# Performance work log

Measured on AMD Instinct MI355X. Metric: run time of the kernel, lower is better.

Reference implementation:

```python
import jax, jax.numpy as jnp
import numpy as np

D_MODEL = 1024
NUM_HEADS = 16
D_K = D_MODEL // NUM_HEADS
THETA = 10000.0


def apply_rope(x, positions):
    # x: [b, h, s, d_k]; positions: [b, s] int32
    half = D_K // 2
    inv_freq = THETA ** (-jnp.arange(half, dtype=jnp.float32) * 2.0 / D_K)  # [half]
    angles = positions[:, None, :, None].astype(jnp.float32) * inv_freq  # [b,1,s,half]
    cos, sin = jnp.cos(angles), jnp.sin(angles)
    x1 = x[..., 0::2]  # even dims
    x2 = x[..., 1::2]  # odd dims
    out_even = x1 * cos - x2 * sin
    out_odd = x1 * sin + x2 * cos
    # re-interleave
    out = jnp.stack([out_even, out_odd], axis=-1)
    return out.reshape(x.shape)


def setup_inputs() -> dict:
    key = jax.random.key(0)
    ks = jax.random.split(key, 5)
    b, s = 2, 2048
    scale = 0.02
    return {
        "x": jax.random.normal(ks[0], (b, s, D_MODEL), dtype=jnp.float32),
        "Wq": jax.random.normal(ks[1], (D_MODEL, D_MODEL), dtype=jnp.float32) * scale,
        "Wk": jax.random.normal(ks[2], (D_MODEL, D_MODEL), dtype=jnp.float32) * scale,
        "Wv": jax.random.normal(ks[3], (D_MODEL, D_MODEL), dtype=jnp.float32) * scale,
        "Wo": jax.random.normal(ks[4], (D_MODEL, D_MODEL), dtype=jnp.float32) * scale,
    }


def reference(x, Wq, Wk, Wv, Wo):
    b, s, _ = x.shape
    # Linear(d, d) applied as x @ W^T (torch Linear convention, no bias)
    Q = x @ Wq.T
    K = x @ Wk.T
    V = x @ Wv.T
    # split heads: [b, s, h*d] -> [b, h, s, d]
    split = lambda t: t.reshape(b, s, NUM_HEADS, D_K).transpose(0, 2, 1, 3)
    Q, K, V = split(Q), split(K), split(V)
    positions = jnp.broadcast_to(jnp.arange(s, dtype=jnp.int32), (b, s))
    Q = apply_rope(Q, positions)
    K = apply_rope(K, positions)
    scores = jnp.einsum('bhqd,bhkd->bhqk', Q, K) / jnp.sqrt(jnp.float32(D_K))
    causal = jnp.tril(jnp.ones((s, s), dtype=bool))
    scores = jnp.where(causal[None, None], scores, -jnp.inf)
    attn = jax.nn.softmax(scores, axis=-1)
    out = jnp.einsum('bhqk,bhkd->bhqd', attn, V)
    out = out.transpose(0, 2, 1, 3).reshape(b, s, D_MODEL)
    return out @ Wo.T
```

## Files before the change

kernel.cpp:

```cpp
#include <hip/hip_runtime.h>

typedef __attribute__((ext_vector_type(8))) short bf16x8;
typedef __attribute__((ext_vector_type(4))) float f32x4;
typedef __attribute__((ext_vector_type(16))) float f32x16;

typedef const __attribute__((address_space(1))) unsigned int gu32;
typedef __attribute__((address_space(3))) unsigned int lu32;

__device__ __forceinline__ void async16(const void* g, void* l) {
  __builtin_amdgcn_global_load_lds((gu32*)g, (lu32*)l, 16, 0, 0);
}

__device__ __forceinline__ unsigned short f2bf(float f) {
  unsigned int u = __float_as_uint(f);
  u += 0x7fffu + ((u >> 16) & 1u);
  return (unsigned short)(u >> 16);
}
__device__ __forceinline__ float b2f(unsigned short s) {
  return __uint_as_float(((unsigned int)s) << 16);
}
__device__ __forceinline__ unsigned int cvtpk(float lo, float hi) {
  unsigned int w;
  asm("v_cvt_pk_bf16_f32 %0, %1, %2" : "=v"(w) : "v"(lo), "v"(hi));
  return w;
}
__device__ __forceinline__ void plswap(unsigned int& x, unsigned int& y) {
  asm("v_permlane32_swap_b32 %0, %1" : "+v"(x), "+v"(y));
}

__global__ __launch_bounds__(256) void cvt_k(const float* __restrict__ in,
                                             unsigned short* __restrict__ out,
                                             int n4) {
  int i = blockIdx.x * 256 + threadIdx.x;
  if (i >= n4) return;
  float4 v = ((const float4*)in)[i];
  ushort4 o;
  o.x = f2bf(v.x); o.y = f2bf(v.y); o.z = f2bf(v.z); o.w = f2bf(v.w);
  ((ushort4*)out)[i] = o;
}

template <int WRITE_F32>
__global__ __launch_bounds__(256) void gemm_bt(const unsigned short* __restrict__ A,
                                               const unsigned short* __restrict__ B,
                                               void* __restrict__ Cp, int N, int K) {
  __shared__ __align__(16) unsigned short Al[128 * 64];
  __shared__ __align__(16) unsigned short Bl[128 * 64];
  const int t = threadIdx.x;
  const int w = t >> 6, l = t & 63;
  const int wm = w >> 1, wn = w & 1;
  const int lr = l & 15, lg = l >> 4;
  const long bm = (long)blockIdx.x * 128, bn = (long)blockIdx.y * 128;
  const int srow = t >> 3, scol = (t & 7) * 8;
  f32x4 acc[4][4] = {};
  for (int k0 = 0; k0 < K; k0 += 64) {
    __syncthreads();
    #pragma unroll
    for (int r = 0; r < 4; ++r) {
      int row = r * 32 + srow;
      async16(&A[(bm + row) * (long)K + k0 + scol], &Al[row * 64 + scol]);
      async16(&B[(bn + row) * (long)K + k0 + scol], &Bl[row * 64 + scol]);
    }
    __syncthreads();
    #pragma unroll
    for (int ks = 0; ks < 2; ++ks) {
      bf16x8 af[4], bf[4];
      #pragma unroll
      for (int i = 0; i < 4; ++i) {
        af[i] = *(const bf16x8*)&Al[(wm * 64 + i * 16 + lr) * 64 + ks * 32 + lg * 8];
        bf[i] = *(const bf16x8*)&Bl[(wn * 64 + i * 16 + lr) * 64 + ks * 32 + lg * 8];
      }
      #pragma unroll
      for (int i = 0; i < 4; ++i)
        #pragma unroll
        for (int j = 0; j < 4; ++j)
          acc[i][j] = __builtin_amdgcn_mfma_f32_16x16x32_bf16(af[i], bf[j], acc[i][j], 0, 0, 0);
    }
  }
  #pragma unroll
  for (int i = 0; i < 4; ++i)
    #pragma unroll
    for (int j = 0; j < 4; ++j)
      #pragma unroll
      for (int r = 0; r < 4; ++r) {
        long row = bm + wm * 64 + i * 16 + lg * 4 + r;
        long col = bn + wn * 64 + j * 16 + lr;
        float v = acc[i][j][r];
        if (WRITE_F32) ((float*)Cp)[row * N + col] = v;
        else ((unsigned short*)Cp)[row * N + col] = f2bf(v);
      }
}

__global__ __launch_bounds__(256) void rope_k(unsigned short* __restrict__ QKV) {
  int idx = blockIdx.x * 256 + threadIdx.x;
  int row = idx >> 9;
  int rem = idx & 511;
  int h = rem >> 5;
  int i = rem & 31;
  int s = row & 2047;
  float invf = exp2f((float)i * (-13.287712379549449f / 32.0f));
  float ang = (float)s * invf;
  float sn, cs;
  sincosf(ang, &sn, &cs);
  size_t base = (size_t)row * 3072 + h * 64 + 2 * i;
  #pragma unroll
  for (int qk = 0; qk < 2; ++qk) {
    size_t off = base + (size_t)qk * 1024;
    float x1 = b2f(QKV[off]);
    float x2 = b2f(QKV[off + 1]);
    QKV[off]     = f2bf(x1 * cs - x2 * sn);
    QKV[off + 1] = f2bf(x1 * sn + x2 * cs);
  }
}

__global__ __launch_bounds__(256) void vtr_k(const unsigned short* __restrict__ QKV,
                                             unsigned short* __restrict__ Vt) {
  __shared__ unsigned short tl[64][66];
  const int kt = blockIdx.x;
  const int bh = blockIdx.y;
  const int b = bh >> 4, h = bh & 15;
  const int t = threadIdx.x;
  const int row = t >> 3, c8 = t & 7;
  #pragma unroll
  for (int r = 0; r < 2; ++r) {
    int k = r * 32 + row;
    bf16x8 v = *(const bf16x8*)&QKV[((long)b * 2048 + kt * 64 + k) * 3072 + 2048 + h * 64 + c8 * 8];
    #pragma unroll
    for (int j = 0; j < 8; ++j) tl[c8 * 8 + j][k] = (unsigned short)v[j];
  }
  __syncthreads();
  #pragma unroll
  for (int r = 0; r < 2; ++r) {
    int d = r * 32 + row;
    ushort4 a, bq;
    a.x = tl[d][c8 * 8 + 0]; a.y = tl[d][c8 * 8 + 1];
    a.z = tl[d][c8 * 8 + 2]; a.w = tl[d][c8 * 8 + 3];
    bq.x = tl[d][c8 * 8 + 4]; bq.y = tl[d][c8 * 8 + 5];
    bq.z = tl[d][c8 * 8 + 6]; bq.w = tl[d][c8 * 8 + 7];
    long off = ((long)bh * 64 + d) * 2048 + kt * 64 + c8 * 8;
    *(ushort4*)&Vt[off] = a;
    *(ushort4*)&Vt[off + 4] = bq;
  }
}

__global__ __launch_bounds__(128) void attn_k(const unsigned short* __restrict__ QKV,
                                              const unsigned short* __restrict__ VtG,
                                              unsigned short* __restrict__ O) {
  __shared__ __align__(16) unsigned short Kl[3][64 * 64];
  __shared__ __align__(16) unsigned short Vl[3][64 * 64];
  const int t = threadIdx.x;
  const int w = t >> 6, l = t & 63;
  const int q31 = l & 31, hi = l >> 5;
  const int bh = blockIdx.x;
  const int qt = 31 - (int)blockIdx.y;
  const int b = bh >> 4, h = bh & 15;
  const int Qb = qt * 64;
  const long rowb = (long)b * 2048;
  const int L = 3072;
  const int NT = qt + 1;
  const int srow = t >> 3;
  const int scol = (t & 7) * 8;
  const int scolK = ((t & 7) ^ (srow & 7)) * 8;
  const float cexp = 0.125f * 1.4426950408889634f;

  const int qmy = Qb + 32 * w + q31;
  const long qgrow = rowb + qmy;

  bf16x8 qf[4];
  #pragma unroll
  for (int dk = 0; dk < 4; ++dk)
    qf[dk] = *(const bf16x8*)&QKV[qgrow * L + h * 64 + dk * 16 + hi * 8];

  float m_ = -1e30f, ls = 0.0f;
  f32x16 oa[2];
  #pragma unroll
  for (int dt = 0; dt < 2; ++dt)
    #pragma unroll
    for (int r = 0; r < 16; ++r) oa[dt][r] = 0.0f;

  auto STAGE = [&](int ts) {
    const int bi = ts % 3;
    const long kb = rowb + (long)ts * 64;
    const long vrowb = (long)bh * 64;
    #pragma unroll
    for (int r = 0; r < 4; ++r) {
      int row = r * 16 + srow;
      async16(&QKV[(kb + row) * L + 1024 + h * 64 + scolK], &Kl[bi][row * 64 + scol]);
      async16(&VtG[(vrowb + row) * 2048 + ts * 64 + scolK], &Vl[bi][row * 64 + scol]);
    }
  };

  STAGE(0);
  if (NT > 1) STAGE(1);

  for (int kt = 0; kt < NT; ++kt) {
    const int cur = kt % 3;
    if (kt < NT - 1) asm volatile("s_waitcnt vmcnt(8)" ::: "memory");
    else             asm volatile("s_waitcnt vmcnt(0)" ::: "memory");
    __builtin_amdgcn_s_barrier();
    __builtin_amdgcn_sched_barrier(0);
    if (kt + 2 < NT) STAGE(kt + 2);

    f32x16 st[2];
    #pragma unroll
    for (int kt2 = 0; kt2 < 2; ++kt2)
      #pragma unroll
      for (int r = 0; r < 16; ++r) st[kt2][r] = 0.0f;
    __builtin_amdgcn_s_setprio(1);
    #pragma unroll
    for (int dk = 0; dk < 4; ++dk)
      #pragma unroll
      for (int kt2 = 0; kt2 < 2; ++kt2) {
        int krow = kt2 * 32 + q31;
        bf16x8 kfr = *(const bf16x8*)&Kl[cur][krow * 64 + (((2 * dk + hi) ^ (krow & 7)) * 8)];
        st[kt2] = __builtin_amdgcn_mfma_f32_32x32x16_bf16(kfr, qf[dk], st[kt2], 0, 0, 0);
      }
    __builtin_amdgcn_s_setprio(0);
    if (kt == NT - 1) {
      #pragma unroll
      for (int kt2 = 0; kt2 < 2; ++kt2)
        #pragma unroll
        for (int r = 0; r < 16; ++r) {
          int kg = kt * 64 + kt2 * 32 + (r & 3) + 8 * (r >> 2) + 4 * hi;
          if (kg > qmy) st[kt2][r] = -1e30f;
        }
    }
    float m0[8];
    #pragma unroll
    for (int i = 0; i < 8; ++i)
      m0[i] = fmaxf(fmaxf(st[0][i], st[0][i + 8]), fmaxf(st[1][i], st[1][i + 8]));
    float mt = fmaxf(fmaxf(fmaxf(m0[0], m0[1]), fmaxf(m0[2], m0[3])),
                     fmaxf(fmaxf(m0[4], m0[5]), fmaxf(m0[6], m0[7])));
    mt = fmaxf(mt, __shfl_xor(mt, 32, 64));
    if (__any((mt - m_) * cexp > 8.0f)) {
      float mn = fmaxf(m_, mt);
      float al = __builtin_amdgcn_exp2f((m_ - mn) * cexp);
      m_ = mn;
      ls *= al;
      #pragma unroll
      for (int dt = 0; dt < 2; ++dt)
        #pragma unroll
        for (int r = 0; r < 16; ++r) oa[dt][r] *= al;
    }
    const float mc = m_ * cexp;
    #pragma unroll
    for (int kt2 = 0; kt2 < 2; ++kt2)
      #pragma unroll
      for (int r = 0; r < 16; ++r)
        st[kt2][r] = __builtin_amdgcn_exp2f(fmaf(st[kt2][r], cexp, -mc));
    float s0[8];
    #pragma unroll
    for (int i = 0; i < 8; ++i)
      s0[i] = (st[0][i] + st[0][i + 8]) + (st[1][i] + st[1][i + 8]);
    float rs = ((s0[0] + s0[1]) + (s0[2] + s0[3])) + ((s0[4] + s0[5]) + (s0[6] + s0[7]));
    rs += __shfl_xor(rs, 32, 64);
    ls += rs;
    bf16x8 pfr[4];
    #pragma unroll
    for (int ks = 0; ks < 4; ++ks) {
      int tt = ks >> 1, gX = 2 * (ks & 1), gY = gX + 1;
      unsigned int x1 = cvtpk(st[tt][4 * gX + 0], st[tt][4 * gX + 1]);
      unsigned int y1 = cvtpk(st[tt][4 * gY + 0], st[tt][4 * gY + 1]);
      plswap(x1, y1);
      unsigned int x2 = cvtpk(st[tt][4 * gX + 2], st[tt][4 * gX + 3]);
      unsigned int y2 = cvtpk(st[tt][4 * gY + 2], st[tt][4 * gY + 3]);
      plswap(x2, y2);
      union { unsigned int u[4]; bf16x8 b; } cc;
      cc.u[0] = x1; cc.u[1] = x2; cc.u[2] = y1; cc.u[3] = y2;
      pfr[ks] = cc.b;
    }
    __builtin_amdgcn_s_setprio(1);
    #pragma unroll
    for (int dt = 0; dt < 2; ++dt)
      #pragma unroll
      for (int ks = 0; ks < 4; ++ks) {
        int vrow = dt * 32 + q31;
        bf16x8 vf = *(const bf16x8*)&Vl[cur][vrow * 64 + (((2 * ks + hi) ^ (vrow & 7)) * 8)];
        oa[dt] = __builtin_amdgcn_mfma_f32_32x32x16_bf16(vf, pfr[ks], oa[dt], 0, 0, 0);
      }
    __builtin_amdgcn_s_setprio(0);
  }
  float inv = 1.0f / ls;
  #pragma unroll
  for (int dt = 0; dt < 2; ++dt)
    #pragma unroll
    for (int g = 0; g < 4; ++g) {
      ushort4 o4;
      o4.x = f2bf(oa[dt][4 * g + 0] * inv);
      o4.y = f2bf(oa[dt][4 * g + 1] * inv);
      o4.z = f2bf(oa[dt][4 * g + 2] * inv);
      o4.w = f2bf(oa[dt][4 * g + 3] * inv);
      *(ushort4*)&O[qgrow * 1024 + h * 64 + dt * 32 + 8 * g + 4 * hi] = o4;
    }
}

extern "C" void kernel_launch(void* const* d_in, const int* in_sizes, int n_in,
                              void* d_out, int out_size, void* d_ws, size_t ws_size,
                              hipStream_t stream) {
  const float* x  = (const float*)d_in[0];
  const float* Wq = (const float*)d_in[1];
  const float* Wk = (const float*)d_in[2];
  const float* Wv = (const float*)d_in[3];
  const float* Wo = (const float*)d_in[4];
  char* ws = (char*)d_ws;
  unsigned short* xb   = (unsigned short*)(ws);
  unsigned short* Wb   = (unsigned short*)(ws + (8u << 20));
  unsigned short* Wob  = (unsigned short*)(ws + (14u << 20));
  unsigned short* QKVb = (unsigned short*)(ws + (16u << 20));
  unsigned short* Ob   = (unsigned short*)(ws + (40u << 20));
  unsigned short* Vtg  = xb;

  cvt_k<<<4096, 256, 0, stream>>>(x, xb, 4096 * 1024 / 4);
  cvt_k<<<1024, 256, 0, stream>>>(Wq, Wb, 1024 * 1024 / 4);
  cvt_k<<<1024, 256, 0, stream>>>(Wk, Wb + 1024 * 1024, 1024 * 1024 / 4);
  cvt_k<<<1024, 256, 0, stream>>>(Wv, Wb + 2 * 1024 * 1024, 1024 * 1024 / 4);
  cvt_k<<<1024, 256, 0, stream>>>(Wo, Wob, 1024 * 1024 / 4);

  gemm_bt<0><<<dim3(32, 24), 256, 0, stream>>>(xb, Wb, QKVb, 3072, 1024);
  rope_k<<<(4096 * 512) / 256, 256, 0, stream>>>(QKVb);
  vtr_k<<<dim3(32, 32), 256, 0, stream>>>(QKVb, Vtg);
  attn_k<<<dim3(32, 32), 128, 0, stream>>>(QKVb, Vtg, Ob);
  gemm_bt<1><<<dim3(32, 8), 256, 0, stream>>>(Ob, Wob, d_out, 1024, 1024);
}
```

Measured before the change: 151.1 us.

## Double-buffer GEMM LDS tiles and XOR-swizzle layout to avoid bank conflicts

The bf16 GEMM kernel now uses two LDS buffers. The next K-tile's async global-to-LDS load is issued right after the barrier, so it overlaps with the MFMA work on the current tile. The global source column is also XOR-swizzled by row, and the LDS reads use the matching swizzled slot, to reduce LDS bank conflicts on the fragment loads. This doubles the LDS footprint to 64KB per block, which may reduce occupancy.

```diff
diff --git a/kernel.cpp b/kernel.cpp
--- a/kernel.cpp
+++ b/kernel.cpp
@@ -43,31 +43,45 @@
 __global__ __launch_bounds__(256) void gemm_bt(const unsigned short* __restrict__ A,
                                                const unsigned short* __restrict__ B,
                                                void* __restrict__ Cp, int N, int K) {
-  __shared__ __align__(16) unsigned short Al[128 * 64];
-  __shared__ __align__(16) unsigned short Bl[128 * 64];
+  __shared__ __align__(16) unsigned short Al[2][128 * 64];
+  __shared__ __align__(16) unsigned short Bl[2][128 * 64];
   const int t = threadIdx.x;
   const int w = t >> 6, l = t & 63;
   const int wm = w >> 1, wn = w & 1;
   const int lr = l & 15, lg = l >> 4;
   const long bm = (long)blockIdx.x * 128, bn = (long)blockIdx.y * 128;
-  const int srow = t >> 3, scol = (t & 7) * 8;
+  const int srow = t >> 3;
+  const int scol = (t & 7) * 8;
+  const int scolS = ((t & 7) ^ (srow & 7)) * 8;
+  const int KT = K >> 6;
   f32x4 acc[4][4] = {};
-  for (int k0 = 0; k0 < K; k0 += 64) {
-    __syncthreads();
+
+  auto STAGE = [&](int ts) {
+    const int bi = ts & 1;
+    const int k0 = ts * 64;
     #pragma unroll
     for (int r = 0; r < 4; ++r) {
       int row = r * 32 + srow;
-      async16(&A[(bm + row) * (long)K + k0 + scol], &Al[row * 64 + scol]);
-      async16(&B[(bn + row) * (long)K + k0 + scol], &Bl[row * 64 + scol]);
-    }
-    __syncthreads();
+      async16(&A[(bm + row) * (long)K + k0 + scolS], &Al[bi][row * 64 + scol]);
+      async16(&B[(bn + row) * (long)K + k0 + scolS], &Bl[bi][row * 64 + scol]);
+    }
+  };
+
+  STAGE(0);
+  for (int kt = 0; kt < KT; ++kt) {
+    const int cur = kt & 1;
+    asm volatile("s_waitcnt vmcnt(0)" ::: "memory");
+    __builtin_amdgcn_s_barrier();
+    __builtin_amdgcn_sched_barrier(0);
+    if (kt + 1 < KT) STAGE(kt + 1);
     #pragma unroll
     for (int ks = 0; ks < 2; ++ks) {
+      const int slot = ((ks * 4 + lg) ^ (lr & 7)) * 8;
       bf16x8 af[4], bf[4];
       #pragma unroll
       for (int i = 0; i < 4; ++i) {
-        af[i] = *(const bf16x8*)&Al[(wm * 64 + i * 16 + lr) * 64 + ks * 32 + lg * 8];
-        bf[i] = *(const bf16x8*)&Bl[(wn * 64 + i * 16 + lr) * 64 + ks * 32 + lg * 8];
+        af[i] = *(const bf16x8*)&Al[cur][(wm * 64 + i * 16 + lr) * 64 + slot];
+        bf[i] = *(const bf16x8*)&Bl[cur][(wn * 64 + i * 16 + lr) * 64 + slot];
       }
       #pragma unroll
       for (int i = 0; i < 4; ++i)
```

After: 137.4 us. 1.1x faster.
